# Performance work log

Measured on AMD Instinct MI355X. Metric: run time of the kernel, lower is better.

Reference implementation:

```python
import jax, jax.numpy as jnp
import numpy as np

D_MODEL, D_STATE, DT_RANK = 1024, 16, 64
BATCH, SEQLEN = 2, 4096

def setup_inputs() -> dict:
    key = jax.random.key(0)
    ks = jax.random.split(key, 6)
    x = jax.random.normal(ks[0], (BATCH, SEQLEN, D_MODEL), dtype=jnp.float32)
    # A = arange(1..N) repeated per channel; A_log = log(A)
    A = jnp.tile(jnp.arange(1, D_STATE + 1, dtype=jnp.float32)[None, :], (D_MODEL, 1))
    A_log = jnp.log(A)
    D_param = jnp.ones((D_MODEL,), dtype=jnp.float32)
    dt_init_std = DT_RANK ** -0.5
    dt_proj_w = jax.random.uniform(ks[1], (D_MODEL, DT_RANK), minval=-dt_init_std, maxval=dt_init_std, dtype=jnp.float32)
    dt = jnp.exp(jax.random.uniform(ks[2], (D_MODEL,)) * (np.log(0.1) - np.log(0.001)) + np.log(0.001))
    dt_proj_b = dt + jnp.log(-jnp.expm1(-dt))
    x_to_dtBC_w = jax.random.normal(ks[3], (DT_RANK + 2 * D_STATE, D_MODEL), dtype=jnp.float32) * (D_MODEL ** -0.5)
    return {"x": x, "A_log": A_log, "D_param": D_param, "dt_proj_w": dt_proj_w, "dt_proj_b": dt_proj_b, "x_to_dtBC_w": x_to_dtBC_w}

def reference(x, A_log, D_param, dt_proj_w, dt_proj_b, x_to_dtBC_w):
    # x: (B,L,D)
    dtBC = jnp.einsum('bld,ed->ble', x, x_to_dtBC_w)            # (B,L,dt_rank+2N)
    dt_in = dtBC[..., :DT_RANK]
    B_in = dtBC[..., DT_RANK:DT_RANK + D_STATE]                  # (B,L,N)
    C_in = dtBC[..., DT_RANK + D_STATE:]                         # (B,L,N)
    dt = jax.nn.softplus(jnp.einsum('blr,dr->bld', dt_in, dt_proj_w) + dt_proj_b)  # (B,L,D)
    A = -jnp.exp(A_log)                                          # (D,N)
    dA = jnp.exp(dt[..., None] * A[None, None])                  # (B,L,D,N)
    dB = dt[..., None] * B_in[:, :, None, :]                     # (B,L,D,N)
    dBx = dB * x[..., None]                                      # (B,L,D,N)

    def step(h, inputs):
        dA_t, dBx_t, C_t = inputs                                # (B,D,N),(B,D,N),(B,N)
        h = dA_t * h + dBx_t
        y_t = jnp.einsum('bdn,bn->bd', h, C_t)
        return h, y_t

    h0 = jnp.zeros((x.shape[0], D_MODEL, D_STATE), dtype=x.dtype)
    xs = (jnp.swapaxes(dA, 0, 1), jnp.swapaxes(dBx, 0, 1), jnp.swapaxes(C_in, 0, 1))
    _, ys = jax.lax.scan(step, h0, xs)                           # (L,B,D)
    y = jnp.swapaxes(ys, 0, 1) + x * D_param[None, None, :]
    return y
```

## Files before the change

### kernel.cpp

```cpp
#include <hip/hip_runtime.h>

#define D_MODEL 1024
#define D_STATE 16
#define DT_RANK 64
#define BATCH 2
#define SEQLEN 4096
#define NROWS (BATCH * SEQLEN)
#define E_DIM 96
#define CH 32
#define NCH (SEQLEN / CH)

typedef short bf16x8 __attribute__((ext_vector_type(8)));
typedef float f32x4 __attribute__((ext_vector_type(4)));

__global__ __launch_bounds__(256)
void k_prep(const float* __restrict__ Wx, const float* __restrict__ W2,
            unsigned short* __restrict__ Wxbf, float* __restrict__ W2T) {
  const int bid = blockIdx.x;
  if (bid < 384) {
    const int idx = bid * 256 + threadIdx.x;
    const float f = Wx[idx];
    unsigned int u = __float_as_uint(f);
    u = (u + 0x7fffu + ((u >> 16) & 1u)) >> 16;
    Wxbf[idx] = (unsigned short)u;
  } else {
    const int idx = (bid - 384) * 256 + threadIdx.x;
    const int r = idx >> 10;
    const int d = idx & 1023;
    W2T[idx] = W2[(size_t)d * DT_RANK + r];
  }
}

__global__ __launch_bounds__(64)
void k_gemm1(const float* __restrict__ x, const unsigned short* __restrict__ Wxbf,
             float* __restrict__ dtBC) {
  const int lane = threadIdx.x;
  const int m0 = blockIdx.x * 16;
  const int r = lane & 15;
  const int kq = lane >> 4;

  f32x4 acc[6];
  #pragma unroll
  for (int j = 0; j < 6; ++j) acc[j] = (f32x4){0.f, 0.f, 0.f, 0.f};

  const float* xrow = x + (size_t)(m0 + r) * D_MODEL + kq * 8;
  const unsigned short* wbase = Wxbf + (size_t)r * D_MODEL + kq * 8;

  #pragma unroll 2
  for (int k0 = 0; k0 < D_MODEL; k0 += 32) {
    const float4 a0 = *reinterpret_cast<const float4*>(xrow + k0);
    const float4 a1 = *reinterpret_cast<const float4*>(xrow + k0 + 4);
    union { unsigned int u[4]; bf16x8 v; } ua;
    asm("v_cvt_pk_bf16_f32 %0, %1, %2" : "=v"(ua.u[0]) : "v"(a0.x), "v"(a0.y));
    asm("v_cvt_pk_bf16_f32 %0, %1, %2" : "=v"(ua.u[1]) : "v"(a0.z), "v"(a0.w));
    asm("v_cvt_pk_bf16_f32 %0, %1, %2" : "=v"(ua.u[2]) : "v"(a1.x), "v"(a1.y));
    asm("v_cvt_pk_bf16_f32 %0, %1, %2" : "=v"(ua.u[3]) : "v"(a1.z), "v"(a1.w));
    const bf16x8 af = ua.v;
    #pragma unroll
    for (int j = 0; j < 6; ++j) {
      const bf16x8 bf = *reinterpret_cast<const bf16x8*>(
          wbase + (size_t)j * 16 * D_MODEL + k0);
      acc[j] = __builtin_amdgcn_mfma_f32_16x16x32_bf16(af, bf, acc[j], 0, 0, 0);
    }
  }
  #pragma unroll
  for (int j = 0; j < 6; ++j)
    #pragma unroll
    for (int i = 0; i < 4; ++i)
      dtBC[(size_t)(m0 + kq * 4 + i) * E_DIM + j * 16 + r] = acc[j][i];
}

#define G2_ROWS 16

__global__ __launch_bounds__(256)
void k_dt(const float* __restrict__ dtBC, const float* __restrict__ W2T,
          const float* __restrict__ b2, float* __restrict__ dt) {
  const int d = blockIdx.x * 256 + threadIdx.x;
  const int m0 = blockIdx.y * G2_ROWS;
  const float bias = b2[d];
  float acc[G2_ROWS];
  #pragma unroll
  for (int i = 0; i < G2_ROWS; ++i) acc[i] = bias;

  for (int r = 0; r < DT_RANK; ++r) {
    const float w = W2T[(size_t)r * D_MODEL + d];
    #pragma unroll
    for (int i = 0; i < G2_ROWS; ++i)
      acc[i] = fmaf(dtBC[(size_t)(m0 + i) * E_DIM + r], w, acc[i]);
  }
  #pragma unroll
  for (int i = 0; i < G2_ROWS; ++i) {
    const float a = acc[i];
    const float sp = (a > 15.f) ? a : __logf(1.f + __expf(a));
    dt[(size_t)(m0 + i) * D_MODEL + d] = sp;
  }
}

__global__ __launch_bounds__(256)
void k_scanA(const float* __restrict__ dt, const float* __restrict__ x,
             const float* __restrict__ dtBC, const float* __restrict__ A_log,
             float* __restrict__ P, float* __restrict__ U) {
  const int d = blockIdx.x * 256 + threadIdx.x;
  const int c = blockIdx.y;
  const int b = blockIdx.z;
  const int t0 = c * CH;

  __shared__ float sB[CH][D_STATE];
  for (int idx = threadIdx.x; idx < CH * D_STATE; idx += 256) {
    const int t = idx >> 4, n = idx & 15;
    sB[t][n] = dtBC[(size_t)(b * SEQLEN + t0 + t) * E_DIM + DT_RANK + n];
  }
  __syncthreads();

  float Ar[D_STATE];
  #pragma unroll
  for (int q = 0; q < 4; ++q) {
    const float4 v = *reinterpret_cast<const float4*>(
        &A_log[(size_t)d * D_STATE + q * 4]);
    Ar[q * 4 + 0] = -__expf(v.x); Ar[q * 4 + 1] = -__expf(v.y);
    Ar[q * 4 + 2] = -__expf(v.z); Ar[q * 4 + 3] = -__expf(v.w);
  }

  float Pr[D_STATE], Ur[D_STATE];
  #pragma unroll
  for (int n = 0; n < D_STATE; ++n) { Pr[n] = 1.f; Ur[n] = 0.f; }

  const float* dtp = dt + (size_t)(b * SEQLEN + t0) * D_MODEL + d;
  const float* xp  = x  + (size_t)(b * SEQLEN + t0) * D_MODEL + d;

  float dtv = dtp[0];
  float xv  = xp[0];
  for (int t = 0; t < CH; ++t) {
    float dtn = 0.f, xn = 0.f;
    if (t + 1 < CH) {
      dtn = dtp[(size_t)(t + 1) * D_MODEL];
      xn  = xp[(size_t)(t + 1) * D_MODEL];
    }
    const float z = dtv * xv;
    #pragma unroll
    for (int n = 0; n < D_STATE; ++n) {
      const float e = __expf(dtv * Ar[n]);
      Ur[n] = fmaf(e, Ur[n], z * sB[t][n]);
      Pr[n] *= e;
    }
    dtv = dtn; xv = xn;
  }
  const size_t base = (size_t)(b * NCH + c) * (D_STATE * D_MODEL) + d;
  #pragma unroll
  for (int n = 0; n < D_STATE; ++n) {
    P[base + (size_t)n * D_MODEL] = Pr[n];
    U[base + (size_t)n * D_MODEL] = Ur[n];
  }
}

__global__ __launch_bounds__(256)
void k_scanB(const float* __restrict__ P, const float* __restrict__ U,
             float* __restrict__ hst) {
  const int idx = blockIdx.x * 256 + threadIdx.x;
  const int b = idx >> 14;
  const int nd = idx & 16383;
  float h = 0.f;
  for (int c = 0; c < NCH; ++c) {
    const size_t off = (size_t)(b * NCH + c) * (D_STATE * D_MODEL) + nd;
    hst[off] = h;
    h = fmaf(P[off], h, U[off]);
  }
}

__global__ __launch_bounds__(256)
void k_scanC(const float* __restrict__ dt, const float* __restrict__ x,
             const float* __restrict__ dtBC, const float* __restrict__ A_log,
             const float* __restrict__ Dp, const float* __restrict__ hst,
             float* __restrict__ y) {
  const int d = blockIdx.x * 256 + threadIdx.x;
  const int c = blockIdx.y;
  const int b = blockIdx.z;
  const int t0 = c * CH;

  __shared__ float sBC[CH][2 * D_STATE];
  for (int idx = threadIdx.x; idx < CH * 2 * D_STATE; idx += 256) {
    const int t = idx >> 5, j = idx & 31;
    sBC[t][j] = dtBC[(size_t)(b * SEQLEN + t0 + t) * E_DIM + DT_RANK + j];
  }
  __syncthreads();

  float Ar[D_STATE];
  #pragma unroll
  for (int q = 0; q < 4; ++q) {
    const float4 v = *reinterpret_cast<const float4*>(
        &A_log[(size_t)d * D_STATE + q * 4]);
    Ar[q * 4 + 0] = -__expf(v.x); Ar[q * 4 + 1] = -__expf(v.y);
    Ar[q * 4 + 2] = -__expf(v.z); Ar[q * 4 + 3] = -__expf(v.w);
  }
  const float Dv = Dp[d];

  float h[D_STATE];
  const size_t hbase = (size_t)(b * NCH + c) * (D_STATE * D_MODEL) + d;
  #pragma unroll
  for (int n = 0; n < D_STATE; ++n) h[n] = hst[hbase + (size_t)n * D_MODEL];

  const float* dtp = dt + (size_t)(b * SEQLEN + t0) * D_MODEL + d;
  const float* xp  = x  + (size_t)(b * SEQLEN + t0) * D_MODEL + d;
  float* yp        = y  + (size_t)(b * SEQLEN + t0) * D_MODEL + d;

  float dtv = dtp[0];
  float xv  = xp[0];
  for (int t = 0; t < CH; ++t) {
    float dtn = 0.f, xn = 0.f;
    if (t + 1 < CH) {
      dtn = dtp[(size_t)(t + 1) * D_MODEL];
      xn  = xp[(size_t)(t + 1) * D_MODEL];
    }
    const float z = dtv * xv;
    float acc = 0.f;
    #pragma unroll
    for (int n = 0; n < D_STATE; ++n) {
      const float e = __expf(dtv * Ar[n]);
      h[n] = fmaf(e, h[n], z * sBC[t][n]);
      acc = fmaf(h[n], sBC[t][D_STATE + n], acc);
    }
    yp[(size_t)t * D_MODEL] = fmaf(xv, Dv, acc);
    dtv = dtn; xv = xn;
  }
}

extern "C" void kernel_launch(void* const* d_in, const int* in_sizes, int n_in,
                              void* d_out, int out_size, void* d_ws, size_t ws_size,
                              hipStream_t stream) {
  const float* x     = (const float*)d_in[0];
  const float* A_log = (const float*)d_in[1];
  const float* Dp    = (const float*)d_in[2];
  const float* W2    = (const float*)d_in[3];
  const float* b2    = (const float*)d_in[4];
  const float* Wx    = (const float*)d_in[5];
  float* out = (float*)d_out;

  float* ws = (float*)d_ws;
  float* dtBC  = ws;
  float* dtbuf = ws +   786432;
  float* P     = ws +  9175040;
  float* U     = ws + 13369344;
  float* hst   = ws + 17563648;
  unsigned short* Wxbf = (unsigned short*)hst;
  float* W2T           = hst + 49152;

  hipLaunchKernelGGL(k_prep, dim3(640), dim3(256), 0, stream, Wx, W2, Wxbf, W2T);
  hipLaunchKernelGGL(k_gemm1, dim3(NROWS / 16), dim3(64), 0, stream,
                     x, Wxbf, dtBC);
  hipLaunchKernelGGL(k_dt, dim3(D_MODEL / 256, NROWS / G2_ROWS), dim3(256), 0,
                     stream, dtBC, W2T, b2, dtbuf);
  hipLaunchKernelGGL(k_scanA, dim3(D_MODEL / 256, NCH, BATCH), dim3(256),
                     0, stream, dtbuf, x, dtBC, A_log, P, U);
  hipLaunchKernelGGL(k_scanB, dim3((BATCH * D_STATE * D_MODEL) / 256),
                     dim3(256), 0, stream, P, U, hst);
  hipLaunchKernelGGL(k_scanC, dim3(D_MODEL / 256, NCH, BATCH), dim3(256),
                     0, stream, dtbuf, x, dtBC, A_log, Dp, hst, out);
}
```

Before: 217.5 us.

## Split-K LDS-tiled projection GEMM, larger scan chunks, batched loads in scans

The first projection GEMM now stages bf16 x and weight tiles in shared memory, with four waves per block and a split-K grid whose partial sums a new reduce kernel adds up. The goal is better weight reuse and more parallelism. The scan chunk length doubles from 32 to 64, which halves the P/U/state buffers and the serial cross-chunk pass. The chunk scans load dt and x in double-buffered groups of 8, k_scanB batches its P/U loads, and k_dt processes 32 rows per block. In exchange it adds an extra launch, writes and reads the partial-sum buffers, and launches fewer blocks for scanA/scanC.

```diff
diff --git a/kernel.cpp b/kernel.cpp
--- a/kernel.cpp
+++ b/kernel.cpp
@@ -7,7 +7,7 @@
 #define SEQLEN 4096
 #define NROWS (BATCH * SEQLEN)
 #define E_DIM 96
-#define CH 32
+#define CH 64
 #define NCH (SEQLEN / CH)
 
 typedef short bf16x8 __attribute__((ext_vector_type(8)));
@@ -19,8 +19,7 @@
   const int bid = blockIdx.x;
   if (bid < 384) {
     const int idx = bid * 256 + threadIdx.x;
-    const float f = Wx[idx];
-    unsigned int u = __float_as_uint(f);
+    unsigned int u = __float_as_uint(Wx[idx]);
     u = (u + 0x7fffu + ((u >> 16) & 1u)) >> 16;
     Wxbf[idx] = (unsigned short)u;
   } else {
@@ -31,46 +30,80 @@
   }
 }
 
-__global__ __launch_bounds__(64)
+#define KSPLIT 4
+#define KSEG (D_MODEL / KSPLIT)
+
+__global__ __launch_bounds__(256)
 void k_gemm1(const float* __restrict__ x, const unsigned short* __restrict__ Wxbf,
-             float* __restrict__ dtBC) {
-  const int lane = threadIdx.x;
-  const int m0 = blockIdx.x * 16;
-  const int r = lane & 15;
-  const int kq = lane >> 4;
+             float* __restrict__ parts) {
+  __shared__ unsigned short sXb[64][72];
+  __shared__ unsigned short sWb[96][72];
+  const int tid = threadIdx.x;
+  const int lane = tid & 63, w = tid >> 6;
+  const int r = lane & 15, kq = lane >> 4;
+  const int m0 = blockIdx.x * 64;
+  const int ks0 = blockIdx.y * KSEG;
 
   f32x4 acc[6];
   #pragma unroll
   for (int j = 0; j < 6; ++j) acc[j] = (f32x4){0.f, 0.f, 0.f, 0.f};
 
-  const float* xrow = x + (size_t)(m0 + r) * D_MODEL + kq * 8;
-  const unsigned short* wbase = Wxbf + (size_t)r * D_MODEL + kq * 8;
-
-  #pragma unroll 2
-  for (int k0 = 0; k0 < D_MODEL; k0 += 32) {
-    const float4 a0 = *reinterpret_cast<const float4*>(xrow + k0);
-    const float4 a1 = *reinterpret_cast<const float4*>(xrow + k0 + 4);
-    union { unsigned int u[4]; bf16x8 v; } ua;
-    asm("v_cvt_pk_bf16_f32 %0, %1, %2" : "=v"(ua.u[0]) : "v"(a0.x), "v"(a0.y));
-    asm("v_cvt_pk_bf16_f32 %0, %1, %2" : "=v"(ua.u[1]) : "v"(a0.z), "v"(a0.w));
-    asm("v_cvt_pk_bf16_f32 %0, %1, %2" : "=v"(ua.u[2]) : "v"(a1.x), "v"(a1.y));
-    asm("v_cvt_pk_bf16_f32 %0, %1, %2" : "=v"(ua.u[3]) : "v"(a1.z), "v"(a1.w));
-    const bf16x8 af = ua.v;
-    #pragma unroll
-    for (int j = 0; j < 6; ++j) {
-      const bf16x8 bf = *reinterpret_cast<const bf16x8*>(
-          wbase + (size_t)j * 16 * D_MODEL + k0);
-      acc[j] = __builtin_amdgcn_mfma_f32_16x16x32_bf16(af, bf, acc[j], 0, 0, 0);
-    }
-  }
+  for (int kt = 0; kt < KSEG; kt += 64) {
+    #pragma unroll
+    for (int s = 0; s < 4; ++s) {
+      const int f = s * 256 + tid;
+      const int row = f >> 4, k4 = f & 15;
+      const float4 v = *reinterpret_cast<const float4*>(
+          &x[(size_t)(m0 + row) * D_MODEL + ks0 + kt + k4 * 4]);
+      unsigned int u0, u1;
+      asm("v_cvt_pk_bf16_f32 %0, %1, %2" : "=v"(u0) : "v"(v.x), "v"(v.y));
+      asm("v_cvt_pk_bf16_f32 %0, %1, %2" : "=v"(u1) : "v"(v.z), "v"(v.w));
+      *reinterpret_cast<uint2*>(&sXb[row][k4 * 4]) = make_uint2(u0, u1);
+    }
+    #pragma unroll
+    for (int s = 0; s < 3; ++s) {
+      const int f = s * 256 + tid;
+      const int e = f >> 3, k8 = f & 7;
+      *reinterpret_cast<uint4*>(&sWb[e][k8 * 8]) =
+          *reinterpret_cast<const uint4*>(
+              &Wxbf[(size_t)e * D_MODEL + ks0 + kt + k8 * 8]);
+    }
+    __syncthreads();
+    #pragma unroll
+    for (int ks = 0; ks < 2; ++ks) {
+      const bf16x8 af = *reinterpret_cast<const bf16x8*>(
+          &sXb[w * 16 + r][ks * 32 + kq * 8]);
+      #pragma unroll
+      for (int j = 0; j < 6; ++j) {
+        const bf16x8 bf = *reinterpret_cast<const bf16x8*>(
+            &sWb[j * 16 + r][ks * 32 + kq * 8]);
+        acc[j] = __builtin_amdgcn_mfma_f32_16x16x32_bf16(af, bf, acc[j], 0, 0, 0);
+      }
+    }
+    __syncthreads();
+  }
+  float* op = parts + (size_t)blockIdx.y * (NROWS * E_DIM);
   #pragma unroll
   for (int j = 0; j < 6; ++j)
     #pragma unroll
     for (int i = 0; i < 4; ++i)
-      dtBC[(size_t)(m0 + kq * 4 + i) * E_DIM + j * 16 + r] = acc[j][i];
-}
-
-#define G2_ROWS 16
+      op[(size_t)(m0 + w * 16 + kq * 4 + i) * E_DIM + j * 16 + r] = acc[j][i];
+}
+
+__global__ __launch_bounds__(256)
+void k_reduce(const float* __restrict__ parts, float* __restrict__ dtBC) {
+  const int i = blockIdx.x * 256 + threadIdx.x;
+  const float4* p = reinterpret_cast<const float4*>(parts);
+  float4 a = p[i];
+  #pragma unroll
+  for (int s = 1; s < KSPLIT; ++s) {
+    const float4 b = p[(size_t)s * (NROWS * E_DIM / 4) + i];
+    a.x += b.x; a.y += b.y; a.z += b.z; a.w += b.w;
+  }
+  reinterpret_cast<float4*>(dtBC)[i] = a;
+}
+
+#define G2_ROWS 32
 
 __global__ __launch_bounds__(256)
 void k_dt(const float* __restrict__ dtBC, const float* __restrict__ W2T,
@@ -128,22 +161,34 @@
   const float* dtp = dt + (size_t)(b * SEQLEN + t0) * D_MODEL + d;
   const float* xp  = x  + (size_t)(b * SEQLEN + t0) * D_MODEL + d;
 
-  float dtv = dtp[0];
-  float xv  = xp[0];
-  for (int t = 0; t < CH; ++t) {
-    float dtn = 0.f, xn = 0.f;
-    if (t + 1 < CH) {
-      dtn = dtp[(size_t)(t + 1) * D_MODEL];
-      xn  = xp[(size_t)(t + 1) * D_MODEL];
-    }
-    const float z = dtv * xv;
-    #pragma unroll
-    for (int n = 0; n < D_STATE; ++n) {
-      const float e = __expf(dtv * Ar[n]);
-      Ur[n] = fmaf(e, Ur[n], z * sB[t][n]);
-      Pr[n] *= e;
-    }
-    dtv = dtn; xv = xn;
+  float db[2][8], xb[2][8];
+  #pragma unroll
+  for (int i = 0; i < 8; ++i) {
+    db[0][i] = dtp[(size_t)i * D_MODEL];
+    xb[0][i] = xp[(size_t)i * D_MODEL];
+  }
+  #pragma unroll
+  for (int tile = 0; tile < CH / 8; ++tile) {
+    const int cur = tile & 1;
+    if (tile < CH / 8 - 1) {
+      #pragma unroll
+      for (int i = 0; i < 8; ++i) {
+        db[cur ^ 1][i] = dtp[(size_t)(tile * 8 + 8 + i) * D_MODEL];
+        xb[cur ^ 1][i] = xp[(size_t)(tile * 8 + 8 + i) * D_MODEL];
+      }
+    }
+    #pragma unroll
+    for (int i = 0; i < 8; ++i) {
+      const float dtv = db[cur][i], xv = xb[cur][i];
+      const float z = dtv * xv;
+      const int t = tile * 8 + i;
+      #pragma unroll
+      for (int n = 0; n < D_STATE; ++n) {
+        const float e = __expf(dtv * Ar[n]);
+        Ur[n] = fmaf(e, Ur[n], z * sB[t][n]);
+        Pr[n] *= e;
+      }
+    }
   }
   const size_t base = (size_t)(b * NCH + c) * (D_STATE * D_MODEL) + d;
   #pragma unroll
@@ -160,10 +205,19 @@
   const int b = idx >> 14;
   const int nd = idx & 16383;
   float h = 0.f;
-  for (int c = 0; c < NCH; ++c) {
-    const size_t off = (size_t)(b * NCH + c) * (D_STATE * D_MODEL) + nd;
-    hst[off] = h;
-    h = fmaf(P[off], h, U[off]);
+  for (int c0 = 0; c0 < NCH; c0 += 8) {
+    float p[8], u[8];
+    #pragma unroll
+    for (int i = 0; i < 8; ++i) {
+      const size_t off = (size_t)(b * NCH + c0 + i) * (D_STATE * D_MODEL) + nd;
+      p[i] = P[off]; u[i] = U[off];
+    }
+    #pragma unroll
+    for (int i = 0; i < 8; ++i) {
+      const size_t off = (size_t)(b * NCH + c0 + i) * (D_STATE * D_MODEL) + nd;
+      hst[off] = h;
+      h = fmaf(p[i], h, u[i]);
+    }
   }
 }
 
@@ -203,24 +257,36 @@
   const float* xp  = x  + (size_t)(b * SEQLEN + t0) * D_MODEL + d;
   float* yp        = y  + (size_t)(b * SEQLEN + t0) * D_MODEL + d;
 
-  float dtv = dtp[0];
-  float xv  = xp[0];
-  for (int t = 0; t < CH; ++t) {
-    float dtn = 0.f, xn = 0.f;
-    if (t + 1 < CH) {
-      dtn = dtp[(size_t)(t + 1) * D_MODEL];
-      xn  = xp[(size_t)(t + 1) * D_MODEL];
-    }
-    const float z = dtv * xv;
-    float acc = 0.f;
-    #pragma unroll
-    for (int n = 0; n < D_STATE; ++n) {
-      const float e = __expf(dtv * Ar[n]);
-      h[n] = fmaf(e, h[n], z * sBC[t][n]);
-      acc = fmaf(h[n], sBC[t][D_STATE + n], acc);
-    }
-    yp[(size_t)t * D_MODEL] = fmaf(xv, Dv, acc);
-    dtv = dtn; xv = xn;
+  float db[2][8], xb[2][8];
+  #pragma unroll
+  for (int i = 0; i < 8; ++i) {
+    db[0][i] = dtp[(size_t)i * D_MODEL];
+    xb[0][i] = xp[(size_t)i * D_MODEL];
+  }
+  #pragma unroll
+  for (int tile = 0; tile < CH / 8; ++tile) {
+    const int cur = tile & 1;
+    if (tile < CH / 8 - 1) {
+      #pragma unroll
+      for (int i = 0; i < 8; ++i) {
+        db[cur ^ 1][i] = dtp[(size_t)(tile * 8 + 8 + i) * D_MODEL];
+        xb[cur ^ 1][i] = xp[(size_t)(tile * 8 + 8 + i) * D_MODEL];
+      }
+    }
+    #pragma unroll
+    for (int i = 0; i < 8; ++i) {
+      const float dtv = db[cur][i], xv = xb[cur][i];
+      const float z = dtv * xv;
+      const int t = tile * 8 + i;
+      float acc = 0.f;
+      #pragma unroll
+      for (int n = 0; n < D_STATE; ++n) {
+        const float e = __expf(dtv * Ar[n]);
+        h[n] = fmaf(e, h[n], z * sBC[t][n]);
+        acc = fmaf(h[n], sBC[t][D_STATE + n], acc);
+      }
+      yp[(size_t)t * D_MODEL] = fmaf(xv, Dv, acc);
+    }
   }
 }
 
@@ -239,14 +305,17 @@
   float* dtBC  = ws;
   float* dtbuf = ws +   786432;
   float* P     = ws +  9175040;
-  float* U     = ws + 13369344;
-  float* hst   = ws + 17563648;
+  float* U     = ws + 11272192;
+  float* hst   = ws + 13369344;
+  float* parts = P;
   unsigned short* Wxbf = (unsigned short*)hst;
   float* W2T           = hst + 49152;
 
   hipLaunchKernelGGL(k_prep, dim3(640), dim3(256), 0, stream, Wx, W2, Wxbf, W2T);
-  hipLaunchKernelGGL(k_gemm1, dim3(NROWS / 16), dim3(64), 0, stream,
-                     x, Wxbf, dtBC);
+  hipLaunchKernelGGL(k_gemm1, dim3(NROWS / 64, KSPLIT), dim3(256), 0, stream,
+                     x, Wxbf, parts);
+  hipLaunchKernelGGL(k_reduce, dim3(NROWS * E_DIM / 4 / 256), dim3(256), 0,
+                     stream, parts, dtBC);
   hipLaunchKernelGGL(k_dt, dim3(D_MODEL / 256, NROWS / G2_ROWS), dim3(256), 0,
                      stream, dtBC, W2T, b2, dtbuf);
   hipLaunchKernelGGL(k_scanA, dim3(D_MODEL / 256, NCH, BATCH), dim3(256),
```

Result: slower. 328.4 us (+51.0%).
